# Kernel optimization log

Hardware: AMD Instinct MI355X
Metric: run time of the kernel (lower is better)

## Reference

```python
import jax, jax.numpy as jnp
import numpy as np

NUM_HARMONICS = 64
SAMPLE_RATE = 48000
TWO_PI = 2.0 * np.pi


def setup_inputs() -> dict:
    key = jax.random.key(0)
    k1, k2, k3 = jax.random.split(key, 3)
    B, N, H = 8, 96000, NUM_HARMONICS
    # f0 in a realistic vocal/instrument range ~ [80, 480] Hz
    f0_hz = 80.0 + 400.0 * jax.random.uniform(k1, (B, N), dtype=jnp.float32)
    amp_harm = jax.random.uniform(k2, (B, N, H), dtype=jnp.float32)
    phase = jax.random.normal(k3, (B, H), dtype=jnp.float32)
    return {"f0_hz": f0_hz, "amp_harm": amp_harm, "phase": phase}


def reference(f0_hz, amp_harm, phase):
    # f0_hz: (B, N); amp_harm: (B, N, H); phase: (B, H)
    H = amp_harm.shape[-1]
    omega = (TWO_PI / SAMPLE_RATE) * f0_hz                      # (B, N)
    harm_idx = jnp.arange(1, H + 1, dtype=f0_hz.dtype)          # (H,)
    omega_h = omega[..., None] * harm_idx                       # (B, N, H)
    phases = jnp.cumsum(omega_h, axis=1) + phase[:, None, :]    # (B, N, H)
    y = jnp.einsum('bnh,bnh->bn', amp_harm, jnp.sin(phases))    # (B, N)
    phase_out = jnp.remainder(phases[:, -1, :], TWO_PI)         # (B, H)
    return (y, phase_out)
```

## Files before the change

### kernel.cpp

```cpp
#include <hip/hip_runtime.h>
#include <cstdint>
#include <cstddef>


#define B   8
#define N   96000
#define H   64
#define CH  768
#define NCH 125
#define TM  384
#define GM  2
#define NWV 6
#define PF  4

static_assert(CH * NCH == N, "chunking");
static_assert(TM * GM == CH, "main scan layout");
static_assert(NCH <= 128, "predecessor sum uses 2 loads/lane");

static constexpr double TWO_PI_D     = 6.2831853071795864769252867665590057684;
static constexpr double INV_TWO_PI_D = 1.0 / TWO_PI_D;
static constexpr double OMEGA_D      = TWO_PI_D / 48000.0;

__device__ __forceinline__ float wrap2pi_f(double v) {
  double r = v - TWO_PI_D * floor(v * INV_TWO_PI_D);
  return (float)r;
}

__global__ __launch_bounds__(256) void k_chunk_sums(const float* __restrict__ f0,
                                                    double* __restrict__ csum) {
  const int blk = blockIdx.x;
  const int b = blk / NCH, c = blk - b * NCH;
  const float* p = f0 + (size_t)b * N + (size_t)c * CH;
  const int tid = threadIdx.x;

  double s = 0.0;
#pragma unroll
  for (int j = 0; j < 3; ++j) s += OMEGA_D * (double)p[tid + j * 256];

  for (int off = 32; off > 0; off >>= 1) s += __shfl_down(s, off);

  __shared__ double sw[4];
  const int lane = tid & 63, wv = tid >> 6;
  if (lane == 0) sw[wv] = s;
  __syncthreads();
  if (tid == 0) csum[blk] = sw[0] + sw[1] + sw[2] + sw[3];
}

__global__ __launch_bounds__(TM, 6) void k_main(const float* __restrict__ f0,
                                                const float* __restrict__ amp,
                                                const float* __restrict__ phase,
                                                const double* __restrict__ csum,
                                                float* __restrict__ out) {
  const int blk = blockIdx.x;
  const int b = blk / NCH, c = blk - b * NCH;
  const int tid = threadIdx.x;
  const int lane = tid & 63, wv = tid >> 6;
  const size_t base = (size_t)b * N + (size_t)c * CH;

  __shared__ float  s_w[CH];
  __shared__ double s_warp[NWV];
  __shared__ double s_pre;
  __shared__ double s_last;

  const float2 f0v = reinterpret_cast<const float2*>(f0 + base)[tid];

  const int hq = lane & 15;
  const int sl = lane >> 4;
  const float4* ampb = reinterpret_cast<const float4*>(amp) + base * (H / 4);
  float4 pf[PF];
#pragma unroll
  for (int j = 0; j < PF; ++j) {
    const int nl = j * 24 + (wv << 2) + sl;
    pf[j] = ampb[(size_t)nl * (H / 4) + hq];
  }

  if (wv == 0) {
    double pre = 0.0;
    if (lane < c)      pre  = csum[b * NCH + lane];
    if (lane + 64 < c) pre += csum[b * NCH + lane + 64];
    for (int off = 32; off > 0; off >>= 1) pre += __shfl_xor(pre, off);
    if (lane == 0) s_pre = pre;
  }

  const double l0 = OMEGA_D * (double)f0v.x;
  const double l1 = OMEGA_D * (double)f0v.y;
  const double ts = l0 + l1;

  double x = ts;
#pragma unroll
  for (int off = 1; off < 64; off <<= 1) {
    double y = __shfl_up(x, off);
    if (lane >= off) x += y;
  }
  if (lane == 63) s_warp[wv] = x;
  __syncthreads();
  if (tid == 0) {
    double a = 0.0;
#pragma unroll
    for (int w = 0; w < NWV; ++w) { double t = s_warp[w]; s_warp[w] = a; a += t; }
  }
  __syncthreads();

  const double run = s_pre + s_warp[wv] + (x - ts);
  const double o0 = run + l0;
  const double o1 = o0 + l1;
  s_w[tid * GM + 0] = wrap2pi_f(o0);
  s_w[tid * GM + 1] = wrap2pi_f(o1);
  if (tid == TM - 1) s_last = o1;
  __syncthreads();

  const float m0 = (float)(hq * 4 + 1), m1 = (float)(hq * 4 + 2);
  const float m2 = (float)(hq * 4 + 3), m3 = (float)(hq * 4 + 4);
  const float* phb = phase + b * H;
  const float p0 = phb[hq * 4 + 0], p1 = phb[hq * 4 + 1];
  const float p2 = phb[hq * 4 + 2], p3 = phb[hq * 4 + 3];
  float* yb = out + base;

#pragma unroll
  for (int j = 0; j < PF; ++j) {
    const int nl = j * 24 + (wv << 2) + sl;
    const float w = s_w[nl];
    const float4 a4 = pf[j];
    float acc;
    acc  = a4.x * __sinf(fmaf(w, m0, p0));
    acc += a4.y * __sinf(fmaf(w, m1, p1));
    acc += a4.z * __sinf(fmaf(w, m2, p2));
    acc += a4.w * __sinf(fmaf(w, m3, p3));
    acc += __shfl_xor(acc, 1);
    acc += __shfl_xor(acc, 2);
    acc += __shfl_xor(acc, 4);
    acc += __shfl_xor(acc, 8);
    if (hq == 0) yb[nl] = acc;
  }

#pragma unroll 4
  for (int i0 = PF * 24; i0 < CH; i0 += 24) {
    const int nl = i0 + (wv << 2) + sl;
    const float w = s_w[nl];
    const float4 a4 = ampb[(size_t)nl * (H / 4) + hq];
    float acc;
    acc  = a4.x * __sinf(fmaf(w, m0, p0));
    acc += a4.y * __sinf(fmaf(w, m1, p1));
    acc += a4.z * __sinf(fmaf(w, m2, p2));
    acc += a4.w * __sinf(fmaf(w, m3, p3));
    acc += __shfl_xor(acc, 1);
    acc += __shfl_xor(acc, 2);
    acc += __shfl_xor(acc, 4);
    acc += __shfl_xor(acc, 8);
    if (hq == 0) yb[nl] = acc;
  }

  if (c == NCH - 1 && tid < H) {
    const double arg = s_last * (double)(tid + 1) + (double)phase[b * H + tid];
    double r = arg - TWO_PI_D * floor(arg * INV_TWO_PI_D);
    if (r < 0.0) r += TWO_PI_D;
    if (r >= TWO_PI_D) r -= TWO_PI_D;
    out[(size_t)B * N + b * H + tid] = (float)r;
  }
}

extern "C" void kernel_launch(void* const* d_in, const int* in_sizes, int n_in,
                              void* d_out, int out_size, void* d_ws, size_t ws_size,
                              hipStream_t stream) {
  const float* f0    = (const float*)d_in[0];
  const float* amp   = (const float*)d_in[1];
  const float* phase = (const float*)d_in[2];
  float* out = (float*)d_out;
  double* csum = (double*)d_ws;

  k_chunk_sums<<<B * NCH, 256, 0, stream>>>(f0, csum);
  k_main<<<B * NCH, TM, 0, stream>>>(f0, amp, phase, csum, out);
}
```

Measured before the change: 39.21 us.

## Streaming amp loads, wave-per-chunk prefix sums, and single-barrier scan offsets

Result: slower. 41.20 us (+5.1%).

```diff
diff --git a/kernel.cpp b/kernel.cpp
--- a/kernel.cpp
+++ b/kernel.cpp
@@ -9,13 +9,15 @@
 #define CH  768
 #define NCH 125
 #define TM  384
+#define NWV 6
 #define GM  2
-#define NWV 6
 #define PF  4
 
 static_assert(CH * NCH == N, "chunking");
 static_assert(TM * GM == CH, "main scan layout");
 static_assert(NCH <= 128, "predecessor sum uses 2 loads/lane");
+
+typedef float vf4 __attribute__((ext_vector_type(4)));
 
 static constexpr double TWO_PI_D     = 6.2831853071795864769252867665590057684;
 static constexpr double INV_TWO_PI_D = 1.0 / TWO_PI_D;
@@ -28,22 +30,19 @@
 
 __global__ __launch_bounds__(256) void k_chunk_sums(const float* __restrict__ f0,
                                                     double* __restrict__ csum) {
-  const int blk = blockIdx.x;
-  const int b = blk / NCH, c = blk - b * NCH;
-  const float* p = f0 + (size_t)b * N + (size_t)c * CH;
-  const int tid = threadIdx.x;
+  const int chunk = (blockIdx.x << 2) + (threadIdx.x >> 6);
+  const int lane = threadIdx.x & 63;
+  const int b = chunk / NCH, c = chunk - b * NCH;
+  const vf4* p = reinterpret_cast<const vf4*>(f0 + (size_t)b * N + (size_t)c * CH);
 
   double s = 0.0;
 #pragma unroll
-  for (int j = 0; j < 3; ++j) s += OMEGA_D * (double)p[tid + j * 256];
-
-  for (int off = 32; off > 0; off >>= 1) s += __shfl_down(s, off);
-
-  __shared__ double sw[4];
-  const int lane = tid & 63, wv = tid >> 6;
-  if (lane == 0) sw[wv] = s;
-  __syncthreads();
-  if (tid == 0) csum[blk] = sw[0] + sw[1] + sw[2] + sw[3];
+  for (int j = 0; j < 3; ++j) {
+    const vf4 v = p[lane + j * 64];
+    s += ((double)v.x + (double)v.y) + ((double)v.z + (double)v.w);
+  }
+  for (int off = 32; off > 0; off >>= 1) s += __shfl_xor(s, off);
+  if (lane == 0) csum[chunk] = OMEGA_D * s;
 }
 
 __global__ __launch_bounds__(TM, 6) void k_main(const float* __restrict__ f0,
@@ -58,7 +57,7 @@
   const size_t base = (size_t)b * N + (size_t)c * CH;
 
   __shared__ float  s_w[CH];
-  __shared__ double s_warp[NWV];
+  __shared__ double s_wsum[NWV];
   __shared__ double s_pre;
   __shared__ double s_last;
 
@@ -66,13 +65,21 @@
 
   const int hq = lane & 15;
   const int sl = lane >> 4;
-  const float4* ampb = reinterpret_cast<const float4*>(amp) + base * (H / 4);
-  float4 pf[PF];
+  const vf4* ampb = reinterpret_cast<const vf4*>(amp) + base * (H / 4);
+  vf4 pf[PF];
 #pragma unroll
   for (int j = 0; j < PF; ++j) {
-    const int nl = j * 24 + (wv << 2) + sl;
-    pf[j] = ampb[(size_t)nl * (H / 4) + hq];
+    const int nl = j * (NWV * 4) + (wv << 2) + sl;
+    pf[j] = __builtin_nontemporal_load(&ampb[(size_t)nl * (H / 4) + hq]);
   }
+
+  const double l0 = OMEGA_D * (double)f0v.x;
+  const double l1 = OMEGA_D * (double)f0v.y;
+  const double ts = l0 + l1;
+
+  double s = ts;
+  for (int off = 32; off > 0; off >>= 1) s += __shfl_xor(s, off);
+  if (lane == 0) s_wsum[wv] = s;
 
   if (wv == 0) {
     double pre = 0.0;
@@ -82,26 +89,19 @@
     if (lane == 0) s_pre = pre;
   }
 
-  const double l0 = OMEGA_D * (double)f0v.x;
-  const double l1 = OMEGA_D * (double)f0v.y;
-  const double ts = l0 + l1;
-
   double x = ts;
 #pragma unroll
   for (int off = 1; off < 64; off <<= 1) {
     double y = __shfl_up(x, off);
     if (lane >= off) x += y;
   }
-  if (lane == 63) s_warp[wv] = x;
-  __syncthreads();
-  if (tid == 0) {
-    double a = 0.0;
-#pragma unroll
-    for (int w = 0; w < NWV; ++w) { double t = s_warp[w]; s_warp[w] = a; a += t; }
-  }
   __syncthreads();
 
-  const double run = s_pre + s_warp[wv] + (x - ts);
+  double wavepre = s_pre;
+#pragma unroll
+  for (int w = 0; w < NWV - 1; ++w) if (w < wv) wavepre += s_wsum[w];
+
+  const double run = wavepre + (x - ts);
   const double o0 = run + l0;
   const double o1 = o0 + l1;
   s_w[tid * GM + 0] = wrap2pi_f(o0);
@@ -118,9 +118,9 @@
 
 #pragma unroll
   for (int j = 0; j < PF; ++j) {
-    const int nl = j * 24 + (wv << 2) + sl;
+    const int nl = j * (NWV * 4) + (wv << 2) + sl;
     const float w = s_w[nl];
-    const float4 a4 = pf[j];
+    const vf4 a4 = pf[j];
     float acc;
     acc  = a4.x * __sinf(fmaf(w, m0, p0));
     acc += a4.y * __sinf(fmaf(w, m1, p1));
@@ -134,10 +134,10 @@
   }
 
 #pragma unroll 4
-  for (int i0 = PF * 24; i0 < CH; i0 += 24) {
+  for (int i0 = PF * (NWV * 4); i0 < CH; i0 += NWV * 4) {
     const int nl = i0 + (wv << 2) + sl;
     const float w = s_w[nl];
-    const float4 a4 = ampb[(size_t)nl * (H / 4) + hq];
+    const vf4 a4 = __builtin_nontemporal_load(&ampb[(size_t)nl * (H / 4) + hq]);
     float acc;
     acc  = a4.x * __sinf(fmaf(w, m0, p0));
     acc += a4.y * __sinf(fmaf(w, m1, p1));
@@ -168,6 +168,6 @@
   float* out = (float*)d_out;
   double* csum = (double*)d_ws;
 
-  k_chunk_sums<<<B * NCH, 256, 0, stream>>>(f0, csum);
+  k_chunk_sums<<<(B * NCH) / 4, 256, 0, stream>>>(f0, csum);
   k_main<<<B * NCH, TM, 0, stream>>>(f0, amp, phase, csum, out);
 }
```
